# Kernel optimization log

Hardware: AMD Instinct MI355X
Metric: run time of the kernel (lower is better)

## Reference

```python
import jax, jax.numpy as jnp
import numpy as np

D_MODEL, N, L_MAX, BATCH = 512, 64, 2048, 8


def _hippo_pq_lambda(n):
    # HiPPO-LegS matrix -> NPLR decomposition (numpy, done once at setup)
    i = np.arange(n)
    A = np.sqrt(2 * i + 1)[:, None] * np.sqrt(2 * i + 1)[None, :]
    A = np.tril(A, -1) + np.diag(i + 1.0)
    p0 = 0.5 * np.sqrt(2 * np.arange(1, n + 1) - 1.0)
    q0 = 2.0 * p0
    S = -A + p0[:, None] * q0[None, :]
    lam, V = np.linalg.eig(S)
    Vc = V.conj().T
    p = Vc @ p0.astype(np.complex128)
    q = Vc @ q0.astype(np.complex128)
    return lam, p, q


def _c2r(x):
    return np.stack([x.real, x.imag], axis=-1).astype(np.float32)


def setup_inputs() -> dict:
    key = jax.random.key(0)
    ks = jax.random.split(key, 6)
    lam, p, q = _hippo_pq_lambda(N)
    log_step_scale = float(np.log(0.1) - np.log(0.001))
    xavier_std = (2.0 / (D_MODEL + N)) ** 0.5
    return {
        "u": jax.random.normal(ks[0], (BATCH, L_MAX, D_MODEL), jnp.float32),
        "lam": jnp.asarray(_c2r(lam)),            # (N, 2) complex-as-real
        "p": jnp.asarray(_c2r(p)),                # (N, 2)
        "q": jnp.asarray(_c2r(q)),                # (N, 2)
        "B": jax.random.normal(ks[1], (D_MODEL, N, 2), jnp.float32) * xavier_std,
        "Ct": jax.random.normal(ks[2], (D_MODEL, N, 2), jnp.float32) * xavier_std,
        "D": jnp.ones((D_MODEL,), jnp.float32),
        "log_step": jax.random.uniform(ks[3], (D_MODEL,), jnp.float32) * log_step_scale + float(np.log(0.001)),
        "W": jax.random.normal(ks[4], (D_MODEL, D_MODEL), jnp.float32) / (D_MODEL ** 0.5),
        "b": jnp.zeros((D_MODEL,), jnp.float32),
        "gamma": jnp.ones((D_MODEL,), jnp.float32),
        "beta": jnp.zeros((D_MODEL,), jnp.float32),
    }


def _cplx(x):
    return x[..., 0] + 1j * x[..., 1]


def _s4_kernel(lam, p, q, B, Ct, step, l_max):
    # Generating function of the DPLR SSM kernel evaluated at roots of unity,
    # then inverse FFT -> length-l_max convolution kernel K, shape (d_model, l_max).
    omega = jnp.exp(2j * jnp.pi * jnp.arange(l_max) / l_max)  # (L,)
    a0, a1 = jnp.conj(Ct), jnp.conj(q)   # (d,n), (n,)
    b0, b1 = B, p                        # (d,n), (n,)
    v = jnp.stack([
        a0 * b0,
        a0 * b1[None, :],
        a1[None, :] * b0,
        jnp.broadcast_to((a1 * b1)[None, :], B.shape),
    ])  # (4, d, n)
    f = (2.0 / step)[:, None] * ((1.0 - omega) / (1.0 + omega))[None, :]  # (d, L)
    r = 1.0 / (f[:, :, None] - lam)      # (d, L, n)  -- dominant intermediate
    k = jnp.einsum('kdn,dln->kdl', v, r) # 4 Cauchy dots in one contraction
    at_roots = (2.0 / (1.0 + omega)) * (k[0] - k[1] * (1.0 / (1.0 + k[3])) * k[2])
    return jnp.fft.ifft(at_roots, n=l_max, axis=-1).real  # (d, L)


def _s4_block(u, lam, p, q, B, Ct, D, log_step, W, b, gamma, beta):
    L = u.shape[1]
    K = _s4_kernel(_cplx(lam), _cplx(p), _cplx(q), _cplx(B), _cplx(Ct), jnp.exp(log_step), L)
    # non-circular convolution via zero-padded FFT
    ud = jnp.fft.rfft(jnp.pad(u, ((0, 0), (0, L), (0, 0))), axis=1)   # (b, L+1, d)
    Kd = jnp.fft.rfft(jnp.pad(K, ((0, 0), (0, L))), axis=-1)          # (d, L+1)
    y = jnp.fft.irfft(ud * Kd.T[None], axis=1)[:, :L, :] + D * u      # S4Layer out
    y = jax.nn.gelu(y, approximate=False)                             # nn.GELU (exact)
    y = y @ W.T + b                                                   # nn.Linear
    y = y + u                                                         # Residual
    mu = jnp.mean(y, axis=-1, keepdims=True)                          # LayerNorm (post)
    var = jnp.mean((y - mu) ** 2, axis=-1, keepdims=True)
    return (y - mu) * jax.lax.rsqrt(var + 1e-5) * gamma + beta


def reference(u, lam, p, q, B, Ct, D, log_step, W, b, gamma, beta):
    return _s4_block(u, lam, p, q, B, Ct, D, log_step, W, b, gamma, beta)
```

## Files before the change

kernel.cpp:

```cpp
#include <hip/hip_runtime.h>
#include <math.h>

#define DM 512
#define NS 64
#define LS 2048
#define NB 8
#define LF 4096
#define LSP (LS + (LS>>5))

typedef float2 cf;
using bf16x8 = __attribute__((ext_vector_type(8))) short;
using f32x4  = __attribute__((ext_vector_type(4))) float;

__device__ __forceinline__ cf cmul(cf a, cf b){ return make_float2(a.x*b.x - a.y*b.y, a.x*b.y + a.y*b.x); }
__device__ __forceinline__ cf cadd(cf a, cf b){ return make_float2(a.x+b.x, a.y+b.y); }
__device__ __forceinline__ cf csub(cf a, cf b){ return make_float2(a.x-b.x, a.y-b.y); }
__device__ __forceinline__ cf cconjf(cf a){ return make_float2(a.x, -a.y); }
__device__ __forceinline__ cf cscalef(cf a, float s){ return make_float2(a.x*s, a.y*s); }
__device__ __forceinline__ cf cdiv_fast(cf a, cf b){
  float inv = __builtin_amdgcn_rcpf(b.x*b.x + b.y*b.y);
  return make_float2((a.x*b.x + a.y*b.y)*inv, (a.y*b.x - a.x*b.y)*inv);
}

__device__ __forceinline__ float gelu_f(float x){
  return 0.5f*x*(1.0f + erff(x*0.7071067811865475f));
}

__device__ __forceinline__ ushort f2bf(float x){
  uint u = __float_as_uint(x);
  return (ushort)((u + 0x7fffu + ((u>>16)&1u)) >> 16);
}

__device__ __forceinline__ int lp(int x){ return x + (x >> 5); }

__device__ __forceinline__ float2 f2add(float2 a, float2 b){ return make_float2(a.x+b.x, a.y+b.y); }
__device__ __forceinline__ float2 f2mul(float2 a, float2 b){ return make_float2(a.x*b.x, a.y*b.y); }
__device__ __forceinline__ float2 f2fma(float2 a, float2 b, float2 c){
  return make_float2(fmaf(a.x,b.x,c.x), fmaf(a.y,b.y,c.y));
}
__device__ __forceinline__ float2 splat2(float s){ return make_float2(s,s); }
__device__ __forceinline__ float2 rcp2(float2 a){
  return make_float2(__builtin_amdgcn_rcpf(a.x), __builtin_amdgcn_rcpf(a.y));
}

template<int N, int T, bool INV>
__device__ float2* fft_stockham4tw(float2* a, float2* b, const float2* tw, int tid) {
  float2* src = a; float2* dst = b;
  const float sg = INV ? 1.0f : -1.0f;
  int m = 1;
  while (m * 4 <= N) {
    __syncthreads();
    #pragma unroll
    for (int ii = 0; ii < N/4/T; ii++) {
      int i = tid + ii*T;
      int j = i & ~(m-1);
      float2 c0 = src[i];
      float2 c1 = src[i + N/4];
      float2 c2 = src[i + 2*(N/4)];
      float2 c3 = src[i + 3*(N/4)];
      float2 s02 = cadd(c0,c2), d02 = csub(c0,c2);
      float2 s13 = cadd(c1,c3), d13 = csub(c1,c3);
      float2 jd13 = make_float2(-sg*d13.y, sg*d13.x);
      float2 y0 = cadd(s02, s13);
      float2 y1 = cadd(d02, jd13);
      float2 y2 = csub(s02, s13);
      float2 y3 = csub(d02, jd13);
      float2 w1 = tw[j];
      if (INV) w1.y = -w1.y;
      float2 w2 = cmul(w1, w1);
      float2 w3 = cmul(w2, w1);
      int o = i + 3*j;
      dst[o]       = y0;
      dst[o + m]   = cmul(y1, w1);
      dst[o + 2*m] = cmul(y2, w2);
      dst[o + 3*m] = cmul(y3, w3);
    }
    float2* tswap = src; src = dst; dst = tswap;
    m <<= 2;
  }
  if (m * 2 <= N) {
    __syncthreads();
    #pragma unroll
    for (int ii = 0; ii < N/2/T; ii++) {
      int i = tid + ii*T;
      float2 c0 = src[i], c1 = src[i + N/2];
      dst[i]     = cadd(c0,c1);
      dst[i + m] = csub(c0,c1);
    }
    float2* tswap = src; src = dst; dst = tswap;
    m <<= 1;
  }
  __syncthreads();
  return src;
}

template<int N, int T, bool INV>
__device__ float2* fft_stockham8(float2* a, float2* b, int tid) {
  float2* src = a; float2* dst = b;
  const float base = (INV ? 6.283185307179586f : -6.283185307179586f) / (float)N;
  const float sg = INV ? 1.0f : -1.0f;
  const float C8 = 0.70710678118654752f;
  int m = 1;
  while (m * 8 <= N) {
    __syncthreads();
    #pragma unroll
    for (int ii = 0; ii < N/8/T; ii++) {
      int i = tid + ii*T;
      int j = i & ~(m-1);
      float2 c[8];
      #pragma unroll
      for (int t = 0; t < 8; t++) c[t] = src[lp(i + t*(N/8))];
      float2 s0=cadd(c[0],c[4]), d0=csub(c[0],c[4]);
      float2 s1=cadd(c[1],c[5]), d1=csub(c[1],c[5]);
      float2 s2=cadd(c[2],c[6]), d2=csub(c[2],c[6]);
      float2 s3=cadd(c[3],c[7]), d3=csub(c[3],c[7]);
      float2 t1 = make_float2(C8*(d1.x - sg*d1.y), C8*(d1.y + sg*d1.x));
      float2 t2 = make_float2(-sg*d2.y, sg*d2.x);
      float2 t3 = make_float2(-C8*(d3.x + sg*d3.y), C8*(sg*d3.x - d3.y));
      float2 es=cadd(s0,s2), ed=csub(s0,s2), fs=cadd(s1,s3), fd=csub(s1,s3);
      float2 je = make_float2(-sg*fd.y, sg*fd.x);
      float2 y0=cadd(es,fs), y4=csub(es,fs);
      float2 y2=cadd(ed,je), y6=csub(ed,je);
      float2 os=cadd(d0,t2), od=csub(d0,t2), ps=cadd(t1,t3), pd=csub(t1,t3);
      float2 jo = make_float2(-sg*pd.y, sg*pd.x);
      float2 y1=cadd(os,ps), y5=csub(os,ps);
      float2 y3=cadd(od,jo), y7=csub(od,jo);
      float ang = base*(float)j;
      float sn, cs; __sincosf(ang, &sn, &cs);
      float2 w1 = make_float2(cs, sn);
      float2 w2 = cmul(w1,w1), w3 = cmul(w2,w1), w4 = cmul(w2,w2);
      float2 w5 = cmul(w4,w1), w6 = cmul(w4,w2), w7 = cmul(w4,w3);
      int o = i + 7*j;
      dst[lp(o)]       = y0;
      dst[lp(o + m)]   = cmul(y1,w1);
      dst[lp(o + 2*m)] = cmul(y2,w2);
      dst[lp(o + 3*m)] = cmul(y3,w3);
      dst[lp(o + 4*m)] = cmul(y4,w4);
      dst[lp(o + 5*m)] = cmul(y5,w5);
      dst[lp(o + 6*m)] = cmul(y6,w6);
      dst[lp(o + 7*m)] = cmul(y7,w7);
    }
    float2* tswap = src; src = dst; dst = tswap;
    m <<= 3;
  }
  if (m * 4 <= N) {
    __syncthreads();
    #pragma unroll
    for (int ii = 0; ii < N/4/T; ii++) {
      int i = tid + ii*T;
      int j = i & ~(m-1);
      float2 c0 = src[lp(i)];
      float2 c1 = src[lp(i + N/4)];
      float2 c2 = src[lp(i + 2*(N/4))];
      float2 c3 = src[lp(i + 3*(N/4))];
      float2 s02 = cadd(c0,c2), d02 = csub(c0,c2);
      float2 s13 = cadd(c1,c3), d13 = csub(c1,c3);
      float2 jd13 = make_float2(-sg*d13.y, sg*d13.x);
      float2 y0 = cadd(s02, s13);
      float2 y1 = cadd(d02, jd13);
      float2 y2 = csub(s02, s13);
      float2 y3 = csub(d02, jd13);
      float ang = base * (float)j;
      float sn, cs; __sincosf(ang, &sn, &cs);
      float2 w1 = make_float2(cs, sn);
      float2 w2 = cmul(w1, w1);
      float2 w3 = cmul(w2, w1);
      int o = i + 3*j;
      dst[lp(o)]       = y0;
      dst[lp(o + m)]   = cmul(y1, w1);
      dst[lp(o + 2*m)] = cmul(y2, w2);
      dst[lp(o + 3*m)] = cmul(y3, w3);
    }
    float2* tswap = src; src = dst; dst = tswap;
    m <<= 2;
  }
  if (m * 2 <= N) {
    __syncthreads();
    #pragma unroll
    for (int ii = 0; ii < N/2/T; ii++) {
      int i = tid + ii*T;
      int j = i & ~(m-1);
      float2 c0 = src[lp(i)], c1 = src[lp(i + N/2)];
      float ang = base * (float)j;
      float sn, cs; __sincosf(ang, &sn, &cs);
      float2 sum = cadd(c0,c1), dif = csub(c0,c1);
      dst[lp(i + j)]     = sum;
      dst[lp(i + j + m)] = cmul(dif, make_float2(cs,sn));
    }
    float2* tswap = src; src = dst; dst = tswap;
    m <<= 1;
  }
  __syncthreads();
  return src;
}


__device__ void transpose_body(const float* __restrict__ u, float* __restrict__ ut,
                               int idx, int tid, float* tile)
{
  int t0 = (idx & 63) * 32;
  int d0 = ((idx >> 6) & 15) * 32;
  int b  = idx >> 10;
  int r  = tid >> 3;
  int cb = (tid & 7) * 4;
  float4 v = *reinterpret_cast<const float4*>(&u[((size_t)b*LS + t0 + r)*DM + d0 + cb]);
  tile[r*33 + cb+0] = v.x;
  tile[r*33 + cb+1] = v.y;
  tile[r*33 + cb+2] = v.z;
  tile[r*33 + cb+3] = v.w;
  __syncthreads();
  int d  = tid >> 3;
  int tb = (tid & 7) * 4;
  float4 o;
  o.x = tile[(tb+0)*33 + d];
  o.y = tile[(tb+1)*33 + d];
  o.z = tile[(tb+2)*33 + d];
  o.w = tile[(tb+3)*33 + d];
  *reinterpret_cast<float4*>(&ut[((size_t)b*DM + d0 + d)*LS + t0 + tb]) = o;
}

__device__ void cauchy_body(const float* __restrict__ lam_g, const float* __restrict__ p_g,
                            const float* __restrict__ q_g,   const float* __restrict__ B_g,
                            const float* __restrict__ Ct_g,  const float* __restrict__ logstep_g,
                            float2* __restrict__ at, int idx, int tid, float* tabRaw)
{
  float (*tab)[12] = reinterpret_cast<float(*)[12]>(tabRaw);
  int d     = idx & 511;
  int chunk = idx >> 9;
  float tos = 2.0f / expf(logstep_g[d]);
  float invtos = __builtin_amdgcn_rcpf(tos);

  if (tid < NS) {
    int n = tid;
    float lx = lam_g[2*n], ly = lam_g[2*n+1];
    cf pn   = make_float2(p_g[2*n],   p_g[2*n+1]);
    cf qn   = make_float2(q_g[2*n],   q_g[2*n+1]);
    cf Bdn  = make_float2(B_g[(d*NS+n)*2],  B_g[(d*NS+n)*2+1]);
    cf Cdn  = make_float2(Ct_g[(d*NS+n)*2], Ct_g[(d*NS+n)*2+1]);
    cf a0 = cconjf(Cdn);
    cf a1 = cconjf(qn);
    cf w0 = cmul(a0, Bdn);
    cf w1 = cmul(a0, pn);
    cf w2 = cmul(a1, Bdn);
    cf w3 = cmul(a1, pn);
    tab[n][0] = -lx;  tab[n][1] = ly;   tab[n][2] = lx*lx; tab[n][3] = w0.x;
    tab[n][4] = w0.y; tab[n][5] = w1.x; tab[n][6] = w1.y;  tab[n][7] = w2.x;
    tab[n][8] = w2.y; tab[n][9] = w3.x; tab[n][10] = w3.y; tab[n][11] = 0.f;
  }

  float gg[2];
  #pragma unroll
  for (int h = 0; h < 2; h++) {
    int l = chunk*512 + h*256 + tid;
    float half_ang = 3.14159265358979323846f * (float)l / (float)LS;
    float sn, cs;
    sincosf(half_ang, &sn, &cs);
    gg[h] = tos * (sn / cs);
  }
  float2 g2 = make_float2(gg[0], gg[1]);
  __syncthreads();

  float2 k0x = splat2(0.f), k0y = splat2(0.f);
  float2 k1x = splat2(0.f), k1y = splat2(0.f);
  float2 k2x = splat2(0.f), k2y = splat2(0.f);
  float2 k3x = splat2(0.f), k3y = splat2(0.f);

  #pragma unroll 4
  for (int n = 0; n < NS; n++) {
    float4 t0 = *reinterpret_cast<const float4*>(&tab[n][0]);
    float4 t1 = *reinterpret_cast<const float4*>(&tab[n][4]);
    float4 t2 = *reinterpret_cast<const float4*>(&tab[n][8]);
    float2 e   = f2add(g2, splat2(t0.y));
    float2 mag = f2fma(e, e, splat2(t0.z));
    float2 inv = rcp2(mag);
    float2 rx  = f2mul(splat2(t0.x), inv);
    float2 ry  = f2mul(e, inv);
    k0x = f2fma(splat2(t0.w), rx, k0x);
    k0x = f2fma(splat2(-t1.x), ry, k0x);
    k0y = f2fma(splat2(t0.w), ry, k0y);
    k0y = f2fma(splat2(t1.x), rx, k0y);
    k1x = f2fma(splat2(t1.y), rx, k1x);
    k1x = f2fma(splat2(-t1.z), ry, k1x);
    k1y = f2fma(splat2(t1.y), ry, k1y);
    k1y = f2fma(splat2(t1.z), rx, k1y);
    k2x = f2fma(splat2(t1.w), rx, k2x);
    k2x = f2fma(splat2(-t2.x), ry, k2x);
    k2y = f2fma(splat2(t1.w), ry, k2y);
    k2y = f2fma(splat2(t2.x), rx, k2y);
    k3x = f2fma(splat2(t2.y), rx, k3x);
    k3x = f2fma(splat2(-t2.z), ry, k3x);
    k3y = f2fma(splat2(t2.y), ry, k3y);
    k3y = f2fma(splat2(t2.z), rx, k3y);
  }

  #pragma unroll
  for (int h = 0; h < 2; h++) {
    int l = chunk*512 + h*256 + tid;
    float gv = (h == 0) ? g2.x : g2.y;
    cf k0 = make_float2(h==0?k0x.x:k0x.y, h==0?k0y.x:k0y.y);
    cf k1 = make_float2(h==0?k1x.x:k1x.y, h==0?k1y.x:k1y.y);
    cf k2 = make_float2(h==0?k2x.x:k2x.y, h==0?k2y.x:k2y.y);
    cf k3 = make_float2(h==0?k3x.x:k3x.y, h==0?k3y.x:k3y.y);
    cf t1c = cdiv_fast(cmul(k1, k2), make_float2(1.0f + k3.x, k3.y));
    cf inner = csub(k0, t1c);
    cf c2 = make_float2(1.0f, -gv * invtos);
    at[(size_t)d*LS + l] = cmul(c2, inner);
  }
}

__device__ void wb_body(const float* __restrict__ W, ushort* __restrict__ Wb,
                        int idx, int tid)
{
  int i = (idx*256 + tid)*4;
  float4 v = *reinterpret_cast<const float4*>(W + i);
  uint2 o;
  o.x = (uint)f2bf(v.x) | ((uint)f2bf(v.y) << 16);
  o.y = (uint)f2bf(v.z) | ((uint)f2bf(v.w) << 16);
  *reinterpret_cast<uint2*>(Wb + i) = o;
}

__global__ __launch_bounds__(256) void fused0_kernel(
    const float* __restrict__ u, float* __restrict__ ut,
    const float* __restrict__ lam_g, const float* __restrict__ p_g,
    const float* __restrict__ q_g,   const float* __restrict__ B_g,
    const float* __restrict__ Ct_g,  const float* __restrict__ logstep_g,
    float2* __restrict__ at,
    const float* __restrict__ W, ushort* __restrict__ Wb)
{
  __shared__ float lds[32*33];
  int bid = blockIdx.x;
  int tid = threadIdx.x;
  if (bid < 10240) {
    int g = bid / 5, r = bid % 5;
    if (r < 4) transpose_body(u, ut, g*4 + r, tid, lds);
    else       cauchy_body(lam_g, p_g, q_g, B_g, Ct_g, logstep_g, at, g, tid, lds);
  } else {
    wb_body(W, Wb, bid - 10240, tid);
  }
}

__global__ __launch_bounds__(256) void kfft_kernel(
    const float2* __restrict__ at, float2* __restrict__ Kf)
{
  __shared__ float2 bufA[LSP];
  __shared__ float2 bufB[LSP];
  int tid = threadIdx.x;
  int d0 = blockIdx.x * 2;
  const float2* at0 = at + (size_t)d0*LS;
  const float2* at1 = at0 + LS;
  float2* Kf0 = Kf + (size_t)d0*LF;
  float2* Kf1 = Kf0 + LF;

  #pragma unroll
  for (int s = 0; s < 8; s++) {
    int k = tid + s*256;
    int nk = (LS - k) & (LS - 1);
    cf a0k = at0[k], a0n = at0[nk];
    cf a1k = at1[k], a1n = at1[nk];
    cf H0 = make_float2(0.5f*(a0k.x + a0n.x), 0.5f*(a0k.y - a0n.y));
    cf H1 = make_float2(0.5f*(a1k.x + a1n.x), 0.5f*(a1k.y - a1n.y));
    Kf0[k] = H0;
    Kf1[k] = H1;
    bufA[lp(k)] = make_float2(H0.x - H1.y, H0.y + H1.x);
  }
  float2* res = fft_stockham8<LS, 256, true>(bufA, bufB, tid);
  float2* other = (res == bufA) ? bufB : bufA;
  #pragma unroll
  for (int s = 0; s < 8; s++) {
    int t = tid + s*256;
    float ang = 3.14159265358979323846f * (float)t / (float)LS;
    float sn, cs;
    __sincosf(ang, &sn, &cs);
    cf Kc = cscalef(res[lp(t)], 1.0f/(float)LS);
    other[lp(t)] = cmul(Kc, make_float2(cs, -sn));
  }
  float2* G = fft_stockham8<LS, 256, false>(other, res, tid);
  #pragma unroll
  for (int s = 0; s < 4; s++) {
    int k = tid + s*256;
    int rk = LS - 1 - k;
    cf Gk = G[lp(k)], Gr = G[lp(rk)];
    cf F0 = make_float2(0.5f*(Gk.x + Gr.x), 0.5f*(Gk.y - Gr.y));
    cf F1 = make_float2(0.5f*(Gk.y + Gr.y), 0.5f*(Gr.x - Gk.x));
    Kf0[LS + k]  = F0;
    Kf0[LS + rk] = cconjf(F0);
    Kf1[LS + k]  = F1;
    Kf1[LS + rk] = cconjf(F1);
  }
}

__global__ __launch_bounds__(512) void conv_kernel(
    const float* __restrict__ ut, const float2* __restrict__ Kf,
    const float* __restrict__ Dv, ushort* __restrict__ gb)
{
  __shared__ float2 bufA[LS];
  __shared__ float2 bufB[LS];
  __shared__ float2 twtab[512];
  int tid = threadIdx.x;
  int d0 = blockIdx.x * 2;
  int b  = blockIdx.y;
  const float* u0p = ut + ((size_t)b*DM + d0)*LS;
  const float* u1p = u0p + LS;
  const float2* Kf0 = Kf + (size_t)d0 * LF;
  const float2* Kf1 = Kf0 + LF;

  {
    float ang = -6.283185307179586f * (float)tid / (float)LS;
    float sn, cs; __sincosf(ang, &sn, &cs);
    twtab[tid] = make_float2(cs, sn);
  }

  float u0r[4], u1r[4];
  #pragma unroll
  for (int s = 0; s < 4; s++) {
    int t = tid + s*512;
    u0r[s] = u0p[t]; u1r[s] = u1p[t];
    bufA[t] = make_float2(u0r[s], u1r[s]);
  }

  float2* Z  = fft_stockham4tw<LS, 512, false>(bufA, bufB, twtab, tid);
  float2* Wb = (Z == bufA) ? bufB : bufA;
  #pragma unroll
  for (int s = 0; s < 4; s++) {
    int mq = tid + s*512;
    int mm = (LS - mq) & (LS - 1);
    cf Za = Z[mq], Zb = Z[mm];
    cf U0 = make_float2(0.5f*(Za.x + Zb.x), 0.5f*(Za.y - Zb.y));
    cf U1 = make_float2(0.5f*(Za.y + Zb.y), 0.5f*(Zb.x - Za.x));
    cf Y0 = cmul(U0, Kf0[mq]);
    cf Y1 = cmul(U1, Kf1[mq]);
    Wb[mq] = make_float2(Y0.x - Y1.y, Y0.y + Y1.x);
  }
  float2* A = fft_stockham4tw<LS, 512, true>(Wb, Z, twtab, tid);
  float2 areg[4];
  #pragma unroll
  for (int s = 0; s < 4; s++) areg[s] = A[tid + s*512];

  float2* st = (A == bufA) ? bufB : bufA;
  #pragma unroll
  for (int s = 0; s < 4; s++) {
    int t = tid + s*512;
    float ang = -3.14159265358979323846f * (float)t / (float)LS;
    float sn, cs; __sincosf(ang, &sn, &cs);
    cf z = make_float2(u0r[s], u1r[s]);
    st[t] = cmul(z, make_float2(cs, sn));
  }
  float2* Z2  = fft_stockham4tw<LS, 512, false>(st, A, twtab, tid);
  float2* Wb2 = (Z2 == bufA) ? bufB : bufA;
  #pragma unroll
  for (int s = 0; s < 4; s++) {
    int mq = tid + s*512;
    int mm = LS - 1 - mq;
    cf Za = Z2[mq], Zb = Z2[mm];
    cf U0 = make_float2(0.5f*(Za.x + Zb.x), 0.5f*(Za.y - Zb.y));
    cf U1 = make_float2(0.5f*(Za.y + Zb.y), 0.5f*(Zb.x - Za.x));
    cf Y0 = cmul(U0, Kf0[LS + mq]);
    cf Y1 = cmul(U1, Kf1[LS + mq]);
    Wb2[mq] = make_float2(Y0.x - Y1.y, Y0.y + Y1.x);
  }
  float2* C = fft_stockham4tw<LS, 512, true>(Wb2, Z2, twtab, tid);

  float dv0 = Dv[d0], dv1 = Dv[d0+1];
  ushort* g0 = gb + ((size_t)b*DM + d0)*LS;
  ushort* g1 = g0 + LS;
  #pragma unroll
  for (int s = 0; s < 4; s++) {
    int t = tid + s*512;
    float ang = 3.14159265358979323846f * (float)t / (float)LS;
    float sn, cs; __sincosf(ang, &sn, &cs);
    cf c = C[t];
    cf bb = cmul(c, make_float2(cs, sn));
    float y0 = (areg[s].x + bb.x) * (1.0f/LF) + dv0 * u0r[s];
    float y1 = (areg[s].y + bb.y) * (1.0f/LF) + dv1 * u1r[s];
    g0[t] = f2bf(gelu_f(y0));
    g1[t] = f2bf(gelu_f(y1));
  }
}

#define ASTRIDE 68
__global__ __launch_bounds__(512) void gemm_ln_kernel(
    const ushort* __restrict__ gb, const ushort* __restrict__ Wbm,
    const float* __restrict__ bias, const float* __restrict__ u,
    const float* __restrict__ gamma, const float* __restrict__ beta,
    float* __restrict__ out)
{
  __shared__ ushort Ast[64*ASTRIDE];
  __shared__ ushort Bs[512*64];
  __shared__ float red[2][64][4];
  int tid = threadIdx.x;
  int b  = blockIdx.y;
  int t0 = blockIdx.x * 64;
  int wid = tid >> 6, lane = tid & 63;
  int wm = wid >> 2, wn = wid & 3;
  int m = lane & 15, q = lane >> 4;

  f32x4 acc[2][8];
  #pragma unroll
  for (int i = 0; i < 2; i++)
    #pragma unroll
    for (int j = 0; j < 8; j++)
      acc[i][j] = (f32x4){0.f, 0.f, 0.f, 0.f};

  for (int k0 = 0; k0 < DM; k0 += 64) {
    {
      int r = tid >> 3, g = tid & 7;
      uint4 va = *reinterpret_cast<const uint4*>(gb + ((size_t)b*DM + k0 + r)*LS + t0 + g*8);
      *reinterpret_cast<uint2*>(&Ast[r*ASTRIDE + g*8])     = make_uint2(va.x, va.y);
      *reinterpret_cast<uint2*>(&Ast[r*ASTRIDE + g*8 + 4]) = make_uint2(va.z, va.w);
    }
    #pragma unroll
    for (int i = 0; i < 8; i++) {
      int idx = tid + i*512;
      int r = idx >> 3, g = idx & 7;
      uint4 vb = *reinterpret_cast<const uint4*>(Wbm + (size_t)r*DM + k0 + g*8);
      *reinterpret_cast<uint4*>(&Bs[r*64 + ((g ^ (r&7))*8)]) = vb;
    }
    __syncthreads();
    #pragma unroll
    for (int kk = 0; kk < 64; kk += 32) {
      int gk = (kk >> 3) + q;
      bf16x8 af[2], bfr[8];
      #pragma unroll
      for (int mi = 0; mi < 2; mi++) {
        int trow = wm*32 + mi*16 + m;
        bf16x8 v;
        #pragma unroll
        for (int e = 0; e < 8; e++)
          v[e] = (short)Ast[(gk*8 + e)*ASTRIDE + trow];
        af[mi] = v;
      }
      #pragma unroll
      for (int ni = 0; ni < 8; ni++) {
        int row = wn*128 + ni*16 + m;
        bfr[ni] = *reinterpret_cast<const bf16x8*>(&Bs[row*64 + ((gk ^ (row&7))*8)]);
      }
      #pragma unroll
      for (int mi = 0; mi < 2; mi++)
        #pragma unroll
        for (int ni = 0; ni < 8; ni++)
          acc[mi][ni] = __builtin_amdgcn_mfma_f32_16x16x32_bf16(af[mi], bfr[ni], acc[mi][ni], 0, 0, 0);
    }
    __syncthreads();
  }

  float sum_[2][4], sq_[2][4];
  #pragma unroll
  for (int mi = 0; mi < 2; mi++)
    #pragma unroll
    for (int jj = 0; jj < 4; jj++) { sum_[mi][jj] = 0.f; sq_[mi][jj] = 0.f; }

  #pragma unroll
  for (int mi = 0; mi < 2; mi++) {
    #pragma unroll
    for (int ni = 0; ni < 8; ni++) {
      int col = wn*128 + ni*16 + m;
      float bb = bias[col];
      #pragma unroll
      for (int jj = 0; jj < 4; jj++) {
        int row = t0 + wm*32 + mi*16 + q*4 + jj;
        float y = acc[mi][ni][jj] + bb + u[((size_t)b*LS + row)*DM + col];
        acc[mi][ni][jj] = y;
        sum_[mi][jj] += y;
        sq_[mi][jj]  += y*y;
      }
    }
  }
  #pragma unroll
  for (int mi = 0; mi < 2; mi++)
    #pragma unroll
    for (int jj = 0; jj < 4; jj++) {
      #pragma unroll
      for (int off = 1; off < 16; off <<= 1) {
        sum_[mi][jj] += __shfl_xor(sum_[mi][jj], off, 64);
        sq_[mi][jj]  += __shfl_xor(sq_[mi][jj],  off, 64);
      }
    }
  if (m == 0) {
    #pragma unroll
    for (int mi = 0; mi < 2; mi++)
      #pragma unroll
      for (int jj = 0; jj < 4; jj++) {
        int rowl = wm*32 + mi*16 + q*4 + jj;
        red[0][rowl][wn] = sum_[mi][jj];
        red[1][rowl][wn] = sq_[mi][jj];
      }
  }
  __syncthreads();
  #pragma unroll
  for (int mi = 0; mi < 2; mi++) {
    #pragma unroll
    for (int jj = 0; jj < 4; jj++) {
      int rowl = wm*32 + mi*16 + q*4 + jj;
      float s  = red[0][rowl][0] + red[0][rowl][1] + red[0][rowl][2] + red[0][rowl][3];
      float s2 = red[1][rowl][0] + red[1][rowl][1] + red[1][rowl][2] + red[1][rowl][3];
      float mu  = s * (1.0f/DM);
      float var = s2 * (1.0f/DM) - mu*mu;
      float rs  = rsqrtf(var + 1e-5f);
      int row = t0 + rowl;
      #pragma unroll
      for (int ni = 0; ni < 8; ni++) {
        int col = wn*128 + ni*16 + m;
        size_t off = ((size_t)b*LS + row)*DM + col;
        out[off] = (acc[mi][ni][jj] - mu) * rs * gamma[col] + beta[col];
      }
    }
  }
}

extern "C" void kernel_launch(void* const* d_in, const int* in_sizes, int n_in,
                              void* d_out, int out_size, void* d_ws, size_t ws_size,
                              hipStream_t stream) {
  const float* u       = (const float*)d_in[0];
  const float* lam     = (const float*)d_in[1];
  const float* p       = (const float*)d_in[2];
  const float* q       = (const float*)d_in[3];
  const float* B       = (const float*)d_in[4];
  const float* Ct      = (const float*)d_in[5];
  const float* Dv      = (const float*)d_in[6];
  const float* logstep = (const float*)d_in[7];
  const float* W       = (const float*)d_in[8];
  const float* bias    = (const float*)d_in[9];
  const float* gamma   = (const float*)d_in[10];
  const float* beta    = (const float*)d_in[11];
  float* out = (float*)d_out;

  char* wsb = (char*)d_ws;
  float2* Kf  = (float2*)wsb;
  ushort* gb  = (ushort*)(wsb + (size_t)16*1024*1024);
  float2* at  = (float2*)(wsb + (size_t)32*1024*1024);
  ushort* Wbm = (ushort*)(wsb + (size_t)40*1024*1024);
  float* ut = (float*)d_out;

  fused0_kernel<<<dim3(10496), 256, 0, stream>>>(u, ut, lam, p, q, B, Ct, logstep, at, W, Wbm);
  kfft_kernel<<<dim3(DM/2), 256, 0, stream>>>(at, Kf);
  conv_kernel<<<dim3(DM/2, NB), 512, 0, stream>>>(ut, Kf, Dv, gb);
  gemm_ln_kernel<<<dim3(LS/64, NB), 512, 0, stream>>>(gb, Wbm, bias, u, gamma, beta, out);
}
```

Measured before the change: 137.0 us.

## Fuse first/last FFT radix stages into registers and use 64x64 transpose tiles

```diff
diff --git a/kernel.cpp b/kernel.cpp
--- a/kernel.cpp
+++ b/kernel.cpp
@@ -43,52 +43,72 @@
   return make_float2(__builtin_amdgcn_rcpf(a.x), __builtin_amdgcn_rcpf(a.y));
 }
 
-template<int N, int T, bool INV>
-__device__ float2* fft_stockham4tw(float2* a, float2* b, const float2* tw, int tid) {
-  float2* src = a; float2* dst = b;
+
+template<bool INV>
+__device__ __forceinline__ void reg_stage1(cf c0, cf c1, cf c2, cf c3,
+                                           const float2* tw, int tid, float2* dst)
+{
   const float sg = INV ? 1.0f : -1.0f;
-  int m = 1;
-  while (m * 4 <= N) {
+  float2 s02 = cadd(c0,c2), d02 = csub(c0,c2);
+  float2 s13 = cadd(c1,c3), d13 = csub(c1,c3);
+  float2 jd13 = make_float2(-sg*d13.y, sg*d13.x);
+  float2 y0 = cadd(s02,s13);
+  float2 y1 = cadd(d02,jd13);
+  float2 y2 = csub(s02,s13);
+  float2 y3 = csub(d02,jd13);
+  float2 w1 = tw[tid];
+  if (INV) w1.y = -w1.y;
+  float2 w2 = cmul(w1,w1);
+  float2 w3 = cmul(w2,w1);
+  int o = 4*tid;
+  dst[o]   = y0;
+  dst[o+1] = cmul(y1,w1);
+  dst[o+2] = cmul(y2,w2);
+  dst[o+3] = cmul(y3,w3);
+}
+
+template<bool INV, bool DO_TAIL>
+__device__ float2* fft2048_mid(float2* src, float2* dst, const float2* tw, int tid)
+{
+  const float sg = INV ? 1.0f : -1.0f;
+  #pragma unroll
+  for (int st = 0; st < 4; st++) {
+    int m = 4 << (2*st);
     __syncthreads();
-    #pragma unroll
-    for (int ii = 0; ii < N/4/T; ii++) {
-      int i = tid + ii*T;
-      int j = i & ~(m-1);
-      float2 c0 = src[i];
-      float2 c1 = src[i + N/4];
-      float2 c2 = src[i + 2*(N/4)];
-      float2 c3 = src[i + 3*(N/4)];
-      float2 s02 = cadd(c0,c2), d02 = csub(c0,c2);
-      float2 s13 = cadd(c1,c3), d13 = csub(c1,c3);
-      float2 jd13 = make_float2(-sg*d13.y, sg*d13.x);
-      float2 y0 = cadd(s02, s13);
-      float2 y1 = cadd(d02, jd13);
-      float2 y2 = csub(s02, s13);
-      float2 y3 = csub(d02, jd13);
-      float2 w1 = tw[j];
-      if (INV) w1.y = -w1.y;
-      float2 w2 = cmul(w1, w1);
-      float2 w3 = cmul(w2, w1);
-      int o = i + 3*j;
-      dst[o]       = y0;
-      dst[o + m]   = cmul(y1, w1);
-      dst[o + 2*m] = cmul(y2, w2);
-      dst[o + 3*m] = cmul(y3, w3);
-    }
-    float2* tswap = src; src = dst; dst = tswap;
-    m <<= 2;
-  }
-  if (m * 2 <= N) {
+    int i = tid;
+    int j = i & ~(m-1);
+    float2 c0 = src[i];
+    float2 c1 = src[i + 512];
+    float2 c2 = src[i + 1024];
+    float2 c3 = src[i + 1536];
+    float2 s02 = cadd(c0,c2), d02 = csub(c0,c2);
+    float2 s13 = cadd(c1,c3), d13 = csub(c1,c3);
+    float2 jd13 = make_float2(-sg*d13.y, sg*d13.x);
+    float2 y0 = cadd(s02,s13);
+    float2 y1 = cadd(d02,jd13);
+    float2 y2 = csub(s02,s13);
+    float2 y3 = csub(d02,jd13);
+    float2 w1 = tw[j];
+    if (INV) w1.y = -w1.y;
+    float2 w2 = cmul(w1,w1);
+    float2 w3 = cmul(w2,w1);
+    int o = i + 3*j;
+    dst[o]       = y0;
+    dst[o + m]   = cmul(y1,w1);
+    dst[o + 2*m] = cmul(y2,w2);
+    dst[o + 3*m] = cmul(y3,w3);
+    float2* t2 = src; src = dst; dst = t2;
+  }
+  if (DO_TAIL) {
     __syncthreads();
     #pragma unroll
-    for (int ii = 0; ii < N/2/T; ii++) {
-      int i = tid + ii*T;
-      float2 c0 = src[i], c1 = src[i + N/2];
-      dst[i]     = cadd(c0,c1);
-      dst[i + m] = csub(c0,c1);
-    }
-    float2* tswap = src; src = dst; dst = tswap;
-    m <<= 1;
+    for (int ii = 0; ii < 2; ii++) {
+      int i = tid + ii*512;
+      float2 a = src[i], b = src[i + 1024];
+      dst[i]        = cadd(a,b);
+      dst[i + 1024] = csub(a,b);
+    }
+    float2* t2 = src; src = dst; dst = t2;
   }
   __syncthreads();
   return src;
@@ -195,28 +215,34 @@
 }
 
 
-__device__ void transpose_body(const float* __restrict__ u, float* __restrict__ ut,
-                               int idx, int tid, float* tile)
-{
-  int t0 = (idx & 63) * 32;
-  int d0 = ((idx >> 6) & 15) * 32;
-  int b  = idx >> 10;
-  int r  = tid >> 3;
-  int cb = (tid & 7) * 4;
-  float4 v = *reinterpret_cast<const float4*>(&u[((size_t)b*LS + t0 + r)*DM + d0 + cb]);
-  tile[r*33 + cb+0] = v.x;
-  tile[r*33 + cb+1] = v.y;
-  tile[r*33 + cb+2] = v.z;
-  tile[r*33 + cb+3] = v.w;
+__device__ void transpose_body64(const float* __restrict__ u, float* __restrict__ ut,
+                                 int idx, int tid, float* tile)
+{
+  int t0 = (idx & 31) * 64;
+  int d0 = ((idx >> 5) & 7) * 64;
+  int b  = idx >> 8;
+  int r  = tid >> 4;
+  int cb = (tid & 15) * 4;
+  #pragma unroll
+  for (int it = 0; it < 4; it++) {
+    int rr = r + it*16;
+    float4 v = *reinterpret_cast<const float4*>(&u[((size_t)b*LS + t0 + rr)*DM + d0 + cb]);
+    tile[rr*65 + cb+0] = v.x;
+    tile[rr*65 + cb+1] = v.y;
+    tile[rr*65 + cb+2] = v.z;
+    tile[rr*65 + cb+3] = v.w;
+  }
   __syncthreads();
-  int d  = tid >> 3;
-  int tb = (tid & 7) * 4;
-  float4 o;
-  o.x = tile[(tb+0)*33 + d];
-  o.y = tile[(tb+1)*33 + d];
-  o.z = tile[(tb+2)*33 + d];
-  o.w = tile[(tb+3)*33 + d];
-  *reinterpret_cast<float4*>(&ut[((size_t)b*DM + d0 + d)*LS + t0 + tb]) = o;
+  #pragma unroll
+  for (int it = 0; it < 4; it++) {
+    int dd = r + it*16;
+    float4 o;
+    o.x = tile[(cb+0)*65 + dd];
+    o.y = tile[(cb+1)*65 + dd];
+    o.z = tile[(cb+2)*65 + dd];
+    o.w = tile[(cb+3)*65 + dd];
+    *reinterpret_cast<float4*>(&ut[((size_t)b*DM + d0 + dd)*LS + t0 + cb]) = o;
+  }
 }
 
 __device__ void cauchy_body(const float* __restrict__ lam_g, const float* __restrict__ p_g,
@@ -327,15 +353,15 @@
     float2* __restrict__ at,
     const float* __restrict__ W, ushort* __restrict__ Wb)
 {
-  __shared__ float lds[32*33];
+  __shared__ float lds[64*65];
   int bid = blockIdx.x;
   int tid = threadIdx.x;
-  if (bid < 10240) {
-    int g = bid / 5, r = bid % 5;
-    if (r < 4) transpose_body(u, ut, g*4 + r, tid, lds);
-    else       cauchy_body(lam_g, p_g, q_g, B_g, Ct_g, logstep_g, at, g, tid, lds);
+  if (bid < 4096) {
+    int g = bid >> 1, r = bid & 1;
+    if (r == 0) transpose_body64(u, ut, g, tid, lds);
+    else        cauchy_body(lam_g, p_g, q_g, B_g, Ct_g, logstep_g, at, g, tid, lds);
   } else {
-    wb_body(W, Wb, bid - 10240, tid);
+    wb_body(W, Wb, bid - 4096, tid);
   }
 }
 
@@ -415,11 +441,15 @@
   for (int s = 0; s < 4; s++) {
     int t = tid + s*512;
     u0r[s] = u0p[t]; u1r[s] = u1p[t];
-    bufA[t] = make_float2(u0r[s], u1r[s]);
-  }
-
-  float2* Z  = fft_stockham4tw<LS, 512, false>(bufA, bufB, twtab, tid);
-  float2* Wb = (Z == bufA) ? bufB : bufA;
+  }
+  __syncthreads();
+
+  reg_stage1<false>(make_float2(u0r[0],u1r[0]), make_float2(u0r[1],u1r[1]),
+                    make_float2(u0r[2],u1r[2]), make_float2(u0r[3],u1r[3]),
+                    twtab, tid, bufA);
+  float2* Z = fft2048_mid<false, true>(bufA, bufB, twtab, tid);
+  float2* other = (Z == bufA) ? bufB : bufA;
+  cf yv[4];
   #pragma unroll
   for (int s = 0; s < 4; s++) {
     int mq = tid + s*512;
@@ -429,24 +459,32 @@
     cf U1 = make_float2(0.5f*(Za.y + Zb.y), 0.5f*(Zb.x - Za.x));
     cf Y0 = cmul(U0, Kf0[mq]);
     cf Y1 = cmul(U1, Kf1[mq]);
-    Wb[mq] = make_float2(Y0.x - Y1.y, Y0.y + Y1.x);
-  }
-  float2* A = fft_stockham4tw<LS, 512, true>(Wb, Z, twtab, tid);
-  float2 areg[4];
-  #pragma unroll
-  for (int s = 0; s < 4; s++) areg[s] = A[tid + s*512];
-
-  float2* st = (A == bufA) ? bufB : bufA;
-  #pragma unroll
-  for (int s = 0; s < 4; s++) {
-    int t = tid + s*512;
-    float ang = -3.14159265358979323846f * (float)t / (float)LS;
-    float sn, cs; __sincosf(ang, &sn, &cs);
-    cf z = make_float2(u0r[s], u1r[s]);
-    st[t] = cmul(z, make_float2(cs, sn));
-  }
-  float2* Z2  = fft_stockham4tw<LS, 512, false>(st, A, twtab, tid);
-  float2* Wb2 = (Z2 == bufA) ? bufB : bufA;
+    yv[s] = make_float2(Y0.x - Y1.y, Y0.y + Y1.x);
+  }
+  reg_stage1<true>(yv[0], yv[1], yv[2], yv[3], twtab, tid, other);
+  float2* A5 = fft2048_mid<true, false>(other, Z, twtab, tid);
+  cf areg[4];
+  {
+    cf s0 = A5[tid], s1 = A5[tid+512], s2 = A5[tid+1024], s3 = A5[tid+1536];
+    areg[0] = cadd(s0,s2); areg[1] = cadd(s1,s3);
+    areg[2] = csub(s0,s2); areg[3] = csub(s1,s3);
+  }
+
+  float2* stB = (A5 == bufA) ? bufB : bufA;
+  {
+    cf z[4];
+    #pragma unroll
+    for (int s = 0; s < 4; s++) {
+      int t = tid + s*512;
+      float ang = -3.14159265358979323846f * (float)t / (float)LS;
+      float sn, cs; __sincosf(ang, &sn, &cs);
+      z[s] = cmul(make_float2(u0r[s], u1r[s]), make_float2(cs, sn));
+    }
+    reg_stage1<false>(z[0], z[1], z[2], z[3], twtab, tid, stB);
+  }
+  float2* Z2 = fft2048_mid<false, true>(stB, A5, twtab, tid);
+  float2* other2 = (Z2 == bufA) ? bufB : bufA;
+  cf yv2[4];
   #pragma unroll
   for (int s = 0; s < 4; s++) {
     int mq = tid + s*512;
@@ -456,9 +494,16 @@
     cf U1 = make_float2(0.5f*(Za.y + Zb.y), 0.5f*(Zb.x - Za.x));
     cf Y0 = cmul(U0, Kf0[LS + mq]);
     cf Y1 = cmul(U1, Kf1[LS + mq]);
-    Wb2[mq] = make_float2(Y0.x - Y1.y, Y0.y + Y1.x);
-  }
-  float2* C = fft_stockham4tw<LS, 512, true>(Wb2, Z2, twtab, tid);
+    yv2[s] = make_float2(Y0.x - Y1.y, Y0.y + Y1.x);
+  }
+  reg_stage1<true>(yv2[0], yv2[1], yv2[2], yv2[3], twtab, tid, other2);
+  float2* C5 = fft2048_mid<true, false>(other2, Z2, twtab, tid);
+  cf creg[4];
+  {
+    cf s0 = C5[tid], s1 = C5[tid+512], s2 = C5[tid+1024], s3 = C5[tid+1536];
+    creg[0] = cadd(s0,s2); creg[1] = cadd(s1,s3);
+    creg[2] = csub(s0,s2); creg[3] = csub(s1,s3);
+  }
 
   float dv0 = Dv[d0], dv1 = Dv[d0+1];
   ushort* g0 = gb + ((size_t)b*DM + d0)*LS;
@@ -468,8 +513,7 @@
     int t = tid + s*512;
     float ang = 3.14159265358979323846f * (float)t / (float)LS;
     float sn, cs; __sincosf(ang, &sn, &cs);
-    cf c = C[t];
-    cf bb = cmul(c, make_float2(cs, sn));
+    cf bb = cmul(creg[s], make_float2(cs, sn));
     float y0 = (areg[s].x + bb.x) * (1.0f/LF) + dv0 * u0r[s];
     float y1 = (areg[s].y + bb.y) * (1.0f/LF) + dv1 * u1r[s];
     g0[t] = f2bf(gelu_f(y0));
@@ -631,7 +675,7 @@
   ushort* Wbm = (ushort*)(wsb + (size_t)40*1024*1024);
   float* ut = (float*)d_out;
 
-  fused0_kernel<<<dim3(10496), 256, 0, stream>>>(u, ut, lam, p, q, B, Ct, logstep, at, W, Wbm);
+  fused0_kernel<<<dim3(4352), 256, 0, stream>>>(u, ut, lam, p, q, B, Ct, logstep, at, W, Wbm);
   kfft_kernel<<<dim3(DM/2), 256, 0, stream>>>(at, Kf);
   conv_kernel<<<dim3(DM/2, NB), 512, 0, stream>>>(ut, Kf, Dv, gb);
   gemm_ln_kernel<<<dim3(LS/64, NB), 512, 0, stream>>>(gb, Wbm, bias, u, gamma, beta, out);
```

New measurement: 151.0 us. 1.1x slower.
